# Performance work log

Hardware: AMD Instinct MI355X
Metric: run time of the kernel (lower is better)

Reference implementation:

```python
import jax, jax.numpy as jnp
import numpy as np

B = 131072
NQ = 5
Z = jnp.array([1.0, -1.0], dtype=jnp.float32)


def _axshape(w):
    return [2 if k == w else 1 for k in range(NQ)]


def _apply_1q(state, U, w):
    # state: (B,2,2,2,2,2) complex64; apply 2x2 gate U on qubit w
    st = jnp.moveaxis(state, 1 + w, -1)
    st = st @ U.T
    return jnp.moveaxis(st, -1, 1 + w)


def _rx(t):
    c = jnp.cos(t / 2)
    s = jnp.sin(t / 2)
    return jnp.stack([jnp.stack([c + 0j, -1j * s]), jnp.stack([-1j * s, c + 0j])]).astype(jnp.complex64)


def _ry(t):
    c = jnp.cos(t / 2)
    s = jnp.sin(t / 2)
    return jnp.stack([jnp.stack([c, -s]), jnp.stack([s, c])]).astype(jnp.complex64)


def _quantum(comb, rw):
    # comb: (B,4). Wires 0,1 <- short feats, wire 2 <- 0, wires 3,4 <- long feats.
    zero = jnp.zeros_like(comb[:, 0])
    angles = [comb[:, 0], comb[:, 1], zero, comb[:, 2], comb[:, 3]]
    # RY(a)|0> = [cos(a/2), sin(a/2)] -> batched product state via einsum (B,32)
    qs = [jnp.stack([jnp.cos(a / 2), jnp.sin(a / 2)], -1).astype(jnp.complex64) for a in angles]
    state = jnp.einsum('bi,bj,bk,bl,bm->bijklm', *qs)
    for layer in range(3):
        for i in range(NQ):
            state = _apply_1q(state, _rx(rw[layer, i, 0]), i)
            state = _apply_1q(state, _ry(rw[layer, i, 1]), i)
        for i in range(NQ):
            for j in range(i + 1, NQ):
                # CNOT(i,j) RZ(th,j) CNOT(i,j) == exp(-i th/2 Z_i Z_j): diagonal phase
                zz = Z.reshape(_axshape(i)) * Z.reshape(_axshape(j))
                phase = jnp.exp((-0.5j) * rw[layer, i, j].astype(jnp.complex64) * zz.astype(jnp.complex64))
                state = state * phase[None]
    probs = jnp.real(state * jnp.conj(state))
    ez = [jnp.sum(probs * Z.reshape(_axshape(w))[None], axis=(1, 2, 3, 4, 5)) for w in range(NQ)]
    return jnp.stack(ez, -1)  # (B,5)


def _forward(x_short, x_long, conv_s_w, conv_s_b, lin_s_w, lin_s_b, conv_l_w, conv_l_b, lin_l_w, lin_l_b, reservoir_weights, readout_w, readout_b):
    dn = ('NCH', 'OIH', 'NCH')
    h = jax.lax.conv_general_dilated(x_short, conv_s_w, (1,), [(1, 1)], dimension_numbers=dn) + conv_s_b[None, :, None]
    feat_s = jax.nn.relu(h).reshape(h.shape[0], -1) @ lin_s_w.T + lin_s_b  # (B,2)
    h = jax.lax.conv_general_dilated(x_long, conv_l_w, (1,), [(2, 2)], dimension_numbers=dn) + conv_l_b[None, :, None]
    h = jax.nn.relu(h)
    h = h.reshape(h.shape[0], 4, 10, 2).max(-1)  # MaxPool1d(2): 20 -> 10
    feat_l = h.reshape(h.shape[0], -1) @ lin_l_w.T + lin_l_b  # (B,2)
    comb = jnp.concatenate([feat_s, feat_l], axis=1)  # (B,4)
    qz = _quantum(comb, reservoir_weights)  # (B,5)
    return qz @ readout_w.T + readout_b  # (B,1)


def setup_inputs() -> dict:
    key = jax.random.key(0)
    ks = jax.random.split(key, 12)
    f32 = jnp.float32
    return {
        'x_short': jax.random.normal(ks[0], (B, 1, 5), f32),
        'x_long': jax.random.normal(ks[1], (B, 1, 20), f32),
        'conv_s_w': jax.random.normal(ks[2], (4, 1, 3), f32) * 0.3,
        'conv_s_b': jax.random.normal(ks[3], (4,), f32) * 0.1,
        'lin_s_w': jax.random.normal(ks[4], (2, 20), f32) * 0.15,
        'lin_s_b': jnp.zeros((2,), f32),
        'conv_l_w': jax.random.normal(ks[5], (4, 1, 5), f32) * 0.3,
        'conv_l_b': jax.random.normal(ks[6], (4,), f32) * 0.1,
        'lin_l_w': jax.random.normal(ks[7], (2, 40), f32) * 0.1,
        'lin_l_b': jnp.zeros((2,), f32),
        'reservoir_weights': jax.random.normal(ks[8], (3, 5, 5), f32),
        'readout_w': jax.random.normal(ks[9], (1, 5), f32) * 0.3,
        'readout_b': jnp.zeros((1,), f32),
    }


def reference(x_short, x_long, conv_s_w, conv_s_b, lin_s_w, lin_s_b, conv_l_w, conv_l_b, lin_l_w, lin_l_b, reservoir_weights, readout_w, readout_b):
    return _forward(x_short, x_long, conv_s_w, conv_s_b, lin_s_w, lin_s_b, conv_l_w, conv_l_b, lin_l_w, lin_l_b, reservoir_weights, readout_w, readout_b)
```

## Files before the change

### kernel.cpp

```cpp
#include <hip/hip_runtime.h>
#include <math.h>


__global__ __launch_bounds__(256) void qcr_kernel(
    const float* __restrict__ x_short, const float* __restrict__ x_long,
    const float* __restrict__ conv_s_w, const float* __restrict__ conv_s_b,
    const float* __restrict__ lin_s_w,  const float* __restrict__ lin_s_b,
    const float* __restrict__ conv_l_w, const float* __restrict__ conv_l_b,
    const float* __restrict__ lin_l_w,  const float* __restrict__ lin_l_b,
    const float* __restrict__ rw,       const float* __restrict__ readout_w,
    const float* __restrict__ readout_b, float* __restrict__ out, int nb)
{
    __shared__ float s_rxc[15], s_rxs[15], s_ryc[15], s_rys[15];
    __shared__ float s_zzc[96], s_zzs[96], s_coef[32];

    const int tid = threadIdx.x;

    if (tid < 15) {
        const int l = tid / 5, i = tid % 5;
        const float tx = rw[l*25 + i*5 + 0] * 0.5f;
        const float ty = rw[l*25 + i*5 + 1] * 0.5f;
        s_rxc[tid] = cosf(tx); s_rxs[tid] = sinf(tx);
        s_ryc[tid] = cosf(ty); s_rys[tid] = sinf(ty);
    }
    if (tid >= 32 && tid < 128) {
        const int e = tid - 32;
        const int l = e >> 5, bi = e & 31;
        float ang = 0.f;
        for (int i = 0; i < 5; ++i) {
            const float si = ((bi >> (4 - i)) & 1) ? -1.f : 1.f;
            for (int j = i + 1; j < 5; ++j) {
                const float sj = ((bi >> (4 - j)) & 1) ? -1.f : 1.f;
                ang += rw[l*25 + i*5 + j] * si * sj;
            }
        }
        ang *= -0.5f;
        s_zzc[e] = cosf(ang); s_zzs[e] = sinf(ang);
    }
    if (tid >= 128 && tid < 160) {
        const int bi = tid - 128;
        float c = 0.f;
        for (int w = 0; w < 5; ++w) {
            const float sw = ((bi >> (4 - w)) & 1) ? -1.f : 1.f;
            c += readout_w[w] * sw;
        }
        s_coef[bi] = c;
    }
    __syncthreads();

    const int b = blockIdx.x * 256 + tid;
    if (b >= nb) return;

    float xs[5];
    #pragma unroll
    for (int p = 0; p < 5; ++p) xs[p] = x_short[b*5 + p];

    float f0 = lin_s_b[0], f1 = lin_s_b[1];
    #pragma unroll
    for (int c = 0; c < 4; ++c) {
        #pragma unroll
        for (int p = 0; p < 5; ++p) {
            float h = conv_s_b[c];
            #pragma unroll
            for (int k = 0; k < 3; ++k) {
                const int q = p - 1 + k;
                if (q >= 0 && q < 5) h += conv_s_w[c*3 + k] * xs[q];
            }
            h = fmaxf(h, 0.f);
            f0 += lin_s_w[      c*5 + p] * h;
            f1 += lin_s_w[20 + c*5 + p] * h;
        }
    }

    float xl[20];
    #pragma unroll
    for (int p = 0; p < 20; ++p) xl[p] = x_long[b*20 + p];

    float g0 = lin_l_b[0], g1 = lin_l_b[1];
    #pragma unroll
    for (int c = 0; c < 4; ++c) {
        #pragma unroll
        for (int q = 0; q < 10; ++q) {
            float hm = 0.f;
            #pragma unroll
            for (int t = 0; t < 2; ++t) {
                const int p = 2*q + t;
                float h = conv_l_b[c];
                #pragma unroll
                for (int k = 0; k < 5; ++k) {
                    const int u = p - 2 + k;
                    if (u >= 0 && u < 20) h += conv_l_w[c*5 + k] * xl[u];
                }
                hm = fmaxf(hm, h);
            }
            g0 += lin_l_w[      c*10 + q] * hm;
            g1 += lin_l_w[40 + c*10 + q] * hm;
        }
    }

    float p0c, p0s, p1c, p1s, p3c, p3s, p4c, p4s;
    sincosf(f0 * 0.5f, &p0s, &p0c);
    sincosf(f1 * 0.5f, &p1s, &p1c);
    sincosf(g0 * 0.5f, &p3s, &p3c);
    sincosf(g1 * 0.5f, &p4s, &p4c);

    float ar[32], ai[32];
    #pragma unroll
    for (int idx = 0; idx < 32; ++idx) {
        float v;
        if ((idx >> 2) & 1) {
            v = 0.f;
        } else {
            v = ((idx >> 4) & 1 ? p0s : p0c)
              * ((idx >> 3) & 1 ? p1s : p1c)
              * ((idx >> 1) & 1 ? p3s : p3c)
              * ((idx      ) & 1 ? p4s : p4c);
        }
        ar[idx] = v; ai[idx] = 0.f;
    }

    for (int l = 0; l < 3; ++l) {
        #pragma unroll
        for (int qb = 0; qb < 5; ++qb) {
            const float rc = s_rxc[l*5 + qb], rs = s_rxs[l*5 + qb];
            const float yc = s_ryc[l*5 + qb], ys = s_rys[l*5 + qb];
            const int str = 1 << (4 - qb);
            #pragma unroll
            for (int g = 0; g < 16; ++g) {
                const int i0 = ((g & ~(str - 1)) << 1) | (g & (str - 1));
                const int i1 = i0 | str;
                const float a0r = ar[i0], a0i = ai[i0];
                const float a1r = ar[i1], a1i = ai[i1];
                const float n0r =  rc*a0r + rs*a1i;
                const float n0i =  rc*a0i - rs*a1r;
                const float n1r =  rs*a0i + rc*a1r;
                const float n1i = -rs*a0r + rc*a1i;
                ar[i0] = yc*n0r - ys*n1r;
                ai[i0] = yc*n0i - ys*n1i;
                ar[i1] = ys*n0r + yc*n1r;
                ai[i1] = ys*n0i + yc*n1i;
            }
        }
        #pragma unroll
        for (int idx = 0; idx < 32; ++idx) {
            const float pc = s_zzc[l*32 + idx], ps = s_zzs[l*32 + idx];
            const float r = ar[idx]*pc - ai[idx]*ps;
            ai[idx]       = ar[idx]*ps + ai[idx]*pc;
            ar[idx]       = r;
        }
    }

    float acc = readout_b[0];
    #pragma unroll
    for (int idx = 0; idx < 32; ++idx)
        acc += (ar[idx]*ar[idx] + ai[idx]*ai[idx]) * s_coef[idx];
    out[b] = acc;
}

extern "C" void kernel_launch(void* const* d_in, const int* in_sizes, int n_in,
                              void* d_out, int out_size, void* d_ws, size_t ws_size,
                              hipStream_t stream) {
    const float* x_short    = (const float*)d_in[0];
    const float* x_long     = (const float*)d_in[1];
    const float* conv_s_w   = (const float*)d_in[2];
    const float* conv_s_b   = (const float*)d_in[3];
    const float* lin_s_w    = (const float*)d_in[4];
    const float* lin_s_b    = (const float*)d_in[5];
    const float* conv_l_w   = (const float*)d_in[6];
    const float* conv_l_b   = (const float*)d_in[7];
    const float* lin_l_w    = (const float*)d_in[8];
    const float* lin_l_b    = (const float*)d_in[9];
    const float* rw         = (const float*)d_in[10];
    const float* readout_w  = (const float*)d_in[11];
    const float* readout_b  = (const float*)d_in[12];
    float* out = (float*)d_out;

    const int nb = in_sizes[0] / 5;
    dim3 grid((nb + 255) / 256), block(256);
    hipLaunchKernelGGL(qcr_kernel, grid, block, 0, stream,
                       x_short, x_long, conv_s_w, conv_s_b, lin_s_w, lin_s_b,
                       conv_l_w, conv_l_b, lin_l_w, lin_l_b, rw, readout_w,
                       readout_b, out, nb);
}
```

Before: 98.97 us.

## Precompute quantum circuit as trigonometric polynomial table, evaluate per row

The output is treated as a multilinear trigonometric polynomial in the four input angles, of degree one in cos and sin of each. A single-block setup kernel simulates the circuit at 81 sample angle combinations and converts the samples into 81 coefficients by a separable 3-point transform. The last-layer ZZ phases are dropped because they are diagonal and do not change Z expectations. The per-row kernel then runs only the conv features and a nested FMA evaluation using fast sin and cos, replacing the 32-amplitude statevector simulation per row. This costs an extra launch and reduced-precision trig intrinsics.

```diff
diff --git a/kernel.cpp b/kernel.cpp
--- a/kernel.cpp
+++ b/kernel.cpp
@@ -2,17 +2,13 @@
 #include <math.h>
 
 
-__global__ __launch_bounds__(256) void qcr_kernel(
-    const float* __restrict__ x_short, const float* __restrict__ x_long,
-    const float* __restrict__ conv_s_w, const float* __restrict__ conv_s_b,
-    const float* __restrict__ lin_s_w,  const float* __restrict__ lin_s_b,
-    const float* __restrict__ conv_l_w, const float* __restrict__ conv_l_b,
-    const float* __restrict__ lin_l_w,  const float* __restrict__ lin_l_b,
-    const float* __restrict__ rw,       const float* __restrict__ readout_w,
-    const float* __restrict__ readout_b, float* __restrict__ out, int nb)
+__global__ __launch_bounds__(128) void qcr_setup(
+    const float* __restrict__ rw, const float* __restrict__ readout_w,
+    const float* __restrict__ readout_b, float* __restrict__ T_out)
 {
     __shared__ float s_rxc[15], s_rxs[15], s_ryc[15], s_rys[15];
-    __shared__ float s_zzc[96], s_zzs[96], s_coef[32];
+    __shared__ float s_zzc[64], s_zzs[64], s_coef[32];
+    __shared__ float s_e[81], s_g[81];
 
     const int tid = threadIdx.x;
 
@@ -23,8 +19,8 @@
         s_rxc[tid] = cosf(tx); s_rxs[tid] = sinf(tx);
         s_ryc[tid] = cosf(ty); s_rys[tid] = sinf(ty);
     }
-    if (tid >= 32 && tid < 128) {
-        const int e = tid - 32;
+    if (tid >= 16 && tid < 80) {
+        const int e = tid - 16;
         const int l = e >> 5, bi = e & 31;
         float ang = 0.f;
         for (int i = 0; i < 5; ++i) {
@@ -37,8 +33,8 @@
         ang *= -0.5f;
         s_zzc[e] = cosf(ang); s_zzs[e] = sinf(ang);
     }
-    if (tid >= 128 && tid < 160) {
-        const int bi = tid - 128;
+    if (tid >= 80 && tid < 112) {
+        const int bi = tid - 80;
         float c = 0.f;
         for (int w = 0; w < 5; ++w) {
             const float sw = ((bi >> (4 - w)) & 1) ? -1.f : 1.f;
@@ -48,7 +44,101 @@
     }
     __syncthreads();
 
-    const int b = blockIdx.x * 256 + tid;
+    if (tid < 81) {
+        const int d4 = tid % 3, d3 = (tid / 3) % 3, d1 = (tid / 9) % 3, d0 = tid / 27;
+        const float SH = 0.8660254037844386f;
+        const float p0c = d0==0 ? 1.f : (d0==1 ? 0.5f : -0.5f), p0s = d0==0 ? 0.f : SH;
+        const float p1c = d1==0 ? 1.f : (d1==1 ? 0.5f : -0.5f), p1s = d1==0 ? 0.f : SH;
+        const float p3c = d3==0 ? 1.f : (d3==1 ? 0.5f : -0.5f), p3s = d3==0 ? 0.f : SH;
+        const float p4c = d4==0 ? 1.f : (d4==1 ? 0.5f : -0.5f), p4s = d4==0 ? 0.f : SH;
+
+        float ar[32], ai[32];
+        #pragma unroll
+        for (int idx = 0; idx < 32; ++idx) {
+            float v = 0.f;
+            if (!((idx >> 2) & 1)) {
+                v = ((idx >> 4) & 1 ? p0s : p0c)
+                  * ((idx >> 3) & 1 ? p1s : p1c)
+                  * ((idx >> 1) & 1 ? p3s : p3c)
+                  * ((idx      ) & 1 ? p4s : p4c);
+            }
+            ar[idx] = v; ai[idx] = 0.f;
+        }
+
+        for (int l = 0; l < 3; ++l) {
+            #pragma unroll
+            for (int qb = 0; qb < 5; ++qb) {
+                const float rc = s_rxc[l*5 + qb], rs = s_rxs[l*5 + qb];
+                const float yc = s_ryc[l*5 + qb], ys = s_rys[l*5 + qb];
+                const int str = 1 << (4 - qb);
+                #pragma unroll
+                for (int g = 0; g < 16; ++g) {
+                    const int i0 = ((g & ~(str - 1)) << 1) | (g & (str - 1));
+                    const int i1 = i0 | str;
+                    const float a0r = ar[i0], a0i = ai[i0];
+                    const float a1r = ar[i1], a1i = ai[i1];
+                    const float n0r =  rc*a0r + rs*a1i;
+                    const float n0i =  rc*a0i - rs*a1r;
+                    const float n1r =  rs*a0i + rc*a1r;
+                    const float n1i = -rs*a0r + rc*a1i;
+                    ar[i0] = yc*n0r - ys*n1r;
+                    ai[i0] = yc*n0i - ys*n1i;
+                    ar[i1] = ys*n0r + yc*n1r;
+                    ai[i1] = ys*n0i + yc*n1i;
+                }
+            }
+            if (l < 2) {
+                #pragma unroll
+                for (int idx = 0; idx < 32; ++idx) {
+                    const float pc = s_zzc[l*32 + idx], ps = s_zzs[l*32 + idx];
+                    const float r = ar[idx]*pc - ai[idx]*ps;
+                    ai[idx]       = ar[idx]*ps + ai[idx]*pc;
+                    ar[idx]       = r;
+                }
+            }
+        }
+
+        float acc = readout_b[0];
+        #pragma unroll
+        for (int idx = 0; idx < 32; ++idx)
+            acc += (ar[idx]*ar[idx] + ai[idx]*ai[idx]) * s_coef[idx];
+        s_e[tid] = acc;
+    }
+    __syncthreads();
+
+    #define QCR_PASS(SRC, DST, ST)                                                        \
+        if (tid < 81) {                                                                   \
+            const int ii = (tid / ST) % 3;                                                \
+            const int base = tid - ii * ST;                                               \
+            const float a0 = ii==0 ? (1.f/3.f) : (ii==1 ? (2.f/3.f) : 0.f);               \
+            const float a1 = ii==0 ? (1.f/3.f) : (ii==1 ? (-1.f/3.f) :  0.57735026918962576f); \
+            const float a2 = ii==0 ? (1.f/3.f) : (ii==1 ? (-1.f/3.f) : -0.57735026918962576f); \
+            DST[tid] = a0*SRC[base] + a1*SRC[base+ST] + a2*SRC[base+2*ST];                \
+        }                                                                                 \
+        __syncthreads();
+
+    QCR_PASS(s_e, s_g, 1)
+    QCR_PASS(s_g, s_e, 3)
+    QCR_PASS(s_e, s_g, 9)
+    QCR_PASS(s_g, s_e, 27)
+    #undef QCR_PASS
+
+    if (tid < 81) T_out[tid] = s_e[tid];
+}
+
+__global__ __launch_bounds__(256) void qcr_rows(
+    const float* __restrict__ x_short, const float* __restrict__ x_long,
+    const float* __restrict__ conv_s_w, const float* __restrict__ conv_s_b,
+    const float* __restrict__ lin_s_w,  const float* __restrict__ lin_s_b,
+    const float* __restrict__ conv_l_w, const float* __restrict__ conv_l_b,
+    const float* __restrict__ lin_l_w,  const float* __restrict__ lin_l_b,
+    const float* __restrict__ T_in, float* __restrict__ out, int nb)
+{
+    __shared__ float sT[81];
+    if (threadIdx.x < 81) sT[threadIdx.x] = T_in[threadIdx.x];
+    __syncthreads();
+
+    const int b = blockIdx.x * 256 + threadIdx.x;
     if (b >= nb) return;
 
     float xs[5];
@@ -98,63 +188,28 @@
         }
     }
 
-    float p0c, p0s, p1c, p1s, p3c, p3s, p4c, p4s;
-    sincosf(f0 * 0.5f, &p0s, &p0c);
-    sincosf(f1 * 0.5f, &p1s, &p1c);
-    sincosf(g0 * 0.5f, &p3s, &p3c);
-    sincosf(g1 * 0.5f, &p4s, &p4c);
-
-    float ar[32], ai[32];
-    #pragma unroll
-    for (int idx = 0; idx < 32; ++idx) {
-        float v;
-        if ((idx >> 2) & 1) {
-            v = 0.f;
-        } else {
-            v = ((idx >> 4) & 1 ? p0s : p0c)
-              * ((idx >> 3) & 1 ? p1s : p1c)
-              * ((idx >> 1) & 1 ? p3s : p3c)
-              * ((idx      ) & 1 ? p4s : p4c);
-        }
-        ar[idx] = v; ai[idx] = 0.f;
-    }
-
-    for (int l = 0; l < 3; ++l) {
-        #pragma unroll
-        for (int qb = 0; qb < 5; ++qb) {
-            const float rc = s_rxc[l*5 + qb], rs = s_rxs[l*5 + qb];
-            const float yc = s_ryc[l*5 + qb], ys = s_rys[l*5 + qb];
-            const int str = 1 << (4 - qb);
-            #pragma unroll
-            for (int g = 0; g < 16; ++g) {
-                const int i0 = ((g & ~(str - 1)) << 1) | (g & (str - 1));
-                const int i1 = i0 | str;
-                const float a0r = ar[i0], a0i = ai[i0];
-                const float a1r = ar[i1], a1i = ai[i1];
-                const float n0r =  rc*a0r + rs*a1i;
-                const float n0i =  rc*a0i - rs*a1r;
-                const float n1r =  rs*a0i + rc*a1r;
-                const float n1i = -rs*a0r + rc*a1i;
-                ar[i0] = yc*n0r - ys*n1r;
-                ai[i0] = yc*n0i - ys*n1i;
-                ar[i1] = ys*n0r + yc*n1r;
-                ai[i1] = ys*n0i + yc*n1i;
-            }
-        }
-        #pragma unroll
-        for (int idx = 0; idx < 32; ++idx) {
-            const float pc = s_zzc[l*32 + idx], ps = s_zzs[l*32 + idx];
-            const float r = ar[idx]*pc - ai[idx]*ps;
-            ai[idx]       = ar[idx]*ps + ai[idx]*pc;
-            ar[idx]       = r;
-        }
-    }
-
-    float acc = readout_b[0];
-    #pragma unroll
-    for (int idx = 0; idx < 32; ++idx)
-        acc += (ar[idx]*ar[idx] + ai[idx]*ai[idx]) * s_coef[idx];
-    out[b] = acc;
+    const float c0 = __cosf(f0), sn0 = __sinf(f0);
+    const float c1 = __cosf(f1), sn1 = __sinf(f1);
+    const float c3 = __cosf(g0), sn3 = __sinf(g0);
+    const float c4 = __cosf(g1), sn4 = __sinf(g1);
+
+    float yi[3];
+    #pragma unroll
+    for (int i = 0; i < 3; ++i) {
+        float xj[3];
+        #pragma unroll
+        for (int j = 0; j < 3; ++j) {
+            float wk[3];
+            #pragma unroll
+            for (int k = 0; k < 3; ++k) {
+                const int o = ((i*3 + j)*3 + k)*3;
+                wk[k] = fmaf(sT[o+2], sn4, fmaf(sT[o+1], c4, sT[o]));
+            }
+            xj[j] = fmaf(wk[2], sn3, fmaf(wk[1], c3, wk[0]));
+        }
+        yi[i] = fmaf(xj[2], sn1, fmaf(xj[1], c1, xj[0]));
+    }
+    out[b] = fmaf(yi[2], sn0, fmaf(yi[1], c0, yi[0]));
 }
 
 extern "C" void kernel_launch(void* const* d_in, const int* in_sizes, int n_in,
@@ -174,11 +229,13 @@
     const float* readout_w  = (const float*)d_in[11];
     const float* readout_b  = (const float*)d_in[12];
     float* out = (float*)d_out;
+    float* T   = (float*)d_ws;
 
     const int nb = in_sizes[0] / 5;
-    dim3 grid((nb + 255) / 256), block(256);
-    hipLaunchKernelGGL(qcr_kernel, grid, block, 0, stream,
+
+    hipLaunchKernelGGL(qcr_setup, dim3(1), dim3(128), 0, stream,
+                       rw, readout_w, readout_b, T);
+    hipLaunchKernelGGL(qcr_rows, dim3((nb + 255) / 256), dim3(256), 0, stream,
                        x_short, x_long, conv_s_w, conv_s_b, lin_s_w, lin_s_b,
-                       conv_l_w, conv_l_b, lin_l_w, lin_l_b, rw, readout_w,
-                       readout_b, out, nb);
+                       conv_l_w, conv_l_b, lin_l_w, lin_l_b, T, out, nb);
 }
```

Result: no change. 99.05 us (+0.1%).
